# Kernel tuning notes

Hardware: AMD Instinct MI355X
Metric: run time of the kernel (lower is better)

Reference implementation:

```python
import jax, jax.numpy as jnp
import numpy as np
import math

HEADS = 8
DIM_HEAD = 64
EMB = 512
GROUPS = 32
EPS = 100000.0  # module's literal default norm_eps


def setup_inputs() -> dict:
    key = jax.random.key(0)
    ks = jax.random.split(key, 11)
    B, D, H, W = 2, EMB, 64, 64
    s = 1.0 / math.sqrt(EMB)
    inp = {
        "input": jax.random.normal(ks[0], (B, D, H, W), dtype=jnp.float32),
        "gn_gamma": jnp.ones((EMB,), dtype=jnp.float32),
        "gn_beta": jnp.zeros((EMB,), dtype=jnp.float32),
        "wq": jax.random.normal(ks[1], (EMB, EMB), dtype=jnp.float32) * s,
        "bq": jax.random.normal(ks[2], (EMB,), dtype=jnp.float32) * 0.01,
        "wk": jax.random.normal(ks[3], (EMB, EMB), dtype=jnp.float32) * s,
        "bk": jax.random.normal(ks[4], (EMB,), dtype=jnp.float32) * 0.01,
        "wv": jax.random.normal(ks[5], (EMB, EMB), dtype=jnp.float32) * s,
        "bv": jax.random.normal(ks[6], (EMB,), dtype=jnp.float32) * 0.01,
        "wo": jax.random.normal(ks[7], (EMB, EMB), dtype=jnp.float32) * s,
        "bo": jax.random.normal(ks[8], (EMB,), dtype=jnp.float32) * 0.01,
    }
    return inp


def reference(input, gn_gamma, gn_beta, wq, bq, wk, bk, wv, bv, wo, bo):
    B, D, H, W = input.shape
    S = H * W
    residual = input

    # GroupNorm(32, D) over (C/G, H, W) per group, affine per-channel
    xg = input.reshape(B, GROUPS, (D // GROUPS) * H * W)
    mu = jnp.mean(xg, axis=-1, keepdims=True)
    var = jnp.var(xg, axis=-1, keepdims=True)
    xn = (xg - mu) / jnp.sqrt(var + EPS)
    xn = xn.reshape(B, D, H, W) * gn_gamma[:, None, None] + gn_beta[:, None, None]

    # (B, D, H, W) -> (B, S, D)
    x = xn.reshape(B, D, S).transpose(0, 2, 1)

    # projections (torch Linear: y = x @ W.T + b)
    q = (x @ wq.T + bq).reshape(B, S, HEADS, DIM_HEAD).transpose(0, 2, 1, 3)
    k = (x @ wk.T + bk).reshape(B, S, HEADS, DIM_HEAD).transpose(0, 2, 1, 3)
    v = (x @ wv.T + bv).reshape(B, S, HEADS, DIM_HEAD).transpose(0, 2, 1, 3)

    scale = 1.0 / math.sqrt(DIM_HEAD)
    scores = jnp.einsum("bhqd,bhkd->bhqk", q * scale, k)  # [B, h, S, S]
    attn = jax.nn.softmax(scores, axis=-1)
    o = jnp.einsum("bhqk,bhkd->bhqd", attn, v)  # [B, h, S, dh]
    o = o.transpose(0, 2, 1, 3).reshape(B, S, D)

    out = o @ wo.T + bo  # [B, S, D]
    out = out.transpose(0, 2, 1).reshape(B, D, H, W)
    return out + residual
```

## Files before the change

kernel.cpp:

```cpp
#include <hip/hip_runtime.h>

#define EMB 512
#define SEQ 4096
#define BATCH 2
#define NH 8
#define DH 64
#define GN_EPS 100000.0f
#define ALPHA 0.125f

typedef __bf16 bf16;
typedef __bf16 bf16x8 __attribute__((ext_vector_type(8)));
typedef float f32x4 __attribute__((ext_vector_type(4)));

typedef __attribute__((address_space(1))) unsigned int u32g;
typedef __attribute__((address_space(3))) unsigned int u32l;
__device__ __forceinline__ void gll16(const void* g, void* l) {
  __builtin_amdgcn_global_load_lds((const u32g*)g, (u32l*)l, 16, 0, 0);
}

__global__ __launch_bounds__(256) void stats_k(const float* __restrict__ in,
                                               float* __restrict__ rs,
                                               float* __restrict__ ss) {
  const int row = blockIdx.x;
  const float4* p = (const float4*)(in + (size_t)row * SEQ);
  float s = 0.f, s2 = 0.f;
#pragma unroll
  for (int i = 0; i < 4; ++i) {
    float4 v = p[i * 256 + threadIdx.x];
    s += v.x + v.y + v.z + v.w;
    s2 += v.x * v.x + v.y * v.y + v.z * v.z + v.w * v.w;
  }
#pragma unroll
  for (int o = 32; o > 0; o >>= 1) {
    s += __shfl_down(s, o, 64);
    s2 += __shfl_down(s2, o, 64);
  }
  __shared__ float red[8];
  const int wave = threadIdx.x >> 6, lane = threadIdx.x & 63;
  if (lane == 0) { red[wave] = s; red[4 + wave] = s2; }
  __syncthreads();
  if (threadIdx.x == 0) {
    rs[row] = red[0] + red[1] + red[2] + red[3];
    ss[row] = red[4] + red[5] + red[6] + red[7];
  }
}

__global__ __launch_bounds__(256) void gn_fin_k(const float* __restrict__ rs,
                                                const float* __restrict__ ss,
                                                const float* __restrict__ gamma,
                                                const float* __restrict__ beta,
                                                float* __restrict__ sc,
                                                float* __restrict__ tt,
                                                float* __restrict__ xsum) {
  __shared__ float mus[64], rstds[64];
  const int tid = threadIdx.x;
  if (tid < 64) {
    float s = 0.f, s2 = 0.f;
#pragma unroll
    for (int c = 0; c < 16; ++c) { s += rs[tid * 16 + c]; s2 += ss[tid * 16 + c]; }
    float mu = s * (1.f / 65536.f);
    float var = s2 * (1.f / 65536.f) - mu * mu;
    mus[tid] = mu;
    rstds[tid] = rsqrtf(var + GN_EPS);
  }
  __syncthreads();
  for (int idx = tid; idx < BATCH * EMB; idx += 256) {
    int b = idx >> 9, d = idx & 511;
    int g = b * 32 + (d >> 4);
    float s = rstds[g] * gamma[d];
    float t = beta[d] - mus[g] * s;
    sc[idx] = s;
    tt[idx] = t;
    xsum[idx] = s * rs[idx] + 4096.f * t;
  }
}

__global__ __launch_bounds__(256) void wprep_k(const float* __restrict__ wk, const float* __restrict__ wv,
                                               const float* __restrict__ wo,
                                               const float* __restrict__ bv,
                                               const float* __restrict__ xsum,
                                               bf16* __restrict__ wkb, bf16* __restrict__ wvb,
                                               bf16* __restrict__ wob,
                                               float* __restrict__ kxa, float* __restrict__ vsuma) {
  const int wi = blockIdx.y, b = blockIdx.z;
  if (wi == 2 && b == 1) return;
  const float* W = wi == 0 ? wk : wi == 1 ? wv : wo;
  bf16* WO = wi == 0 ? wkb : wi == 1 ? wvb : wob;
  const int tid = threadIdx.x;
  const int n = blockIdx.x * 64 + (tid >> 2);
  const float* Wr = W + (size_t)n * EMB;
  float dot = 0.f;
  const int dq = (tid & 3) * 128;
  for (int d = dq; d < dq + 128; d += 4) {
    float4 w4 = *(const float4*)&Wr[d];
    if (wi < 2) {
      float4 x4 = *(const float4*)&xsum[b * EMB + d];
      dot += w4.x * x4.x + w4.y * x4.y + w4.z * x4.z + w4.w * x4.w;
    }
    if (b == 0) {
      bf16 r[4] = {(bf16)w4.x, (bf16)w4.y, (bf16)w4.z, (bf16)w4.w};
      *(uint2*)&WO[(size_t)n * EMB + d] = *(uint2*)r;
    }
  }
  if (wi < 2) {
    dot += __shfl_xor(dot, 1, 4);
    dot += __shfl_xor(dot, 2, 4);
    if ((tid & 3) == 0) {
      if (wi == 0) kxa[b * EMB + n] = dot;
      else vsuma[b * EMB + n] = dot + 4096.f * bv[n];
    }
  }
}

__global__ __launch_bounds__(256) void wqt_k(const float* __restrict__ wq,
                                             bf16* __restrict__ wqt) {
  __shared__ float t[64][65];
  const int c0 = blockIdx.x * 64, r0 = blockIdx.y * 64;
  const int tid = threadIdx.x;
#pragma unroll
  for (int p = 0; p < 16; ++p) {
    int lin = p * 256 + tid;
    int rl = lin >> 6, cl = lin & 63;
    t[rl][cl] = wq[(size_t)(r0 + rl) * EMB + c0 + cl];
  }
  __syncthreads();
#pragma unroll
  for (int p = 0; p < 16; ++p) {
    int lin = p * 256 + tid;
    int cl = lin >> 6, rl = lin & 63;
    wqt[(size_t)(c0 + cl) * EMB + r0 + rl] = (bf16)t[rl][cl];
  }
}

__global__ __launch_bounds__(256) void nx_k(const float* __restrict__ in,
                                            const float* __restrict__ sc,
                                            const float* __restrict__ tt,
                                            bf16* __restrict__ xds,
                                            bf16* __restrict__ xsd) {
  __shared__ float t[64][65];
  const int s0 = blockIdx.x * 64, d0 = blockIdx.y * 64, b = blockIdx.z;
  const int tid = threadIdx.x;
#pragma unroll
  for (int p = 0; p < 16; ++p) {
    int lin = p * 256 + tid;
    int dl = lin >> 6, sl = lin & 63;
    int d = d0 + dl;
    size_t idx = ((size_t)b * EMB + d) * SEQ + s0 + sl;
    float v = in[idx] * sc[b * EMB + d] + tt[b * EMB + d];
    t[dl][sl] = v;
    xds[idx] = (bf16)v;
  }
  __syncthreads();
#pragma unroll
  for (int p = 0; p < 16; ++p) {
    int lin = p * 256 + tid;
    int sl = lin >> 6, dl = lin & 63;
    xsd[((size_t)b * SEQ + s0 + sl) * EMB + d0 + dl] = (bf16)t[dl][sl];
  }
}

__global__ __launch_bounds__(256) void graw_k(const bf16* __restrict__ xds,
                                              bf16* __restrict__ G) {
  __shared__ __align__(16) bf16 As[64 * 64];
  __shared__ __align__(16) bf16 Bs[64 * 64];
  const int i0 = blockIdx.x * 64, j0 = blockIdx.y * 64, b = blockIdx.z;
  const bf16* X = xds + (size_t)b * EMB * SEQ;
  const int tid = threadIdx.x;
  const int wave = tid >> 6, lane = tid & 63, l16 = lane & 15, quad = lane >> 4;
  const int lr = lane >> 3, lc = (lane & 7) << 3;
  f32x4 acc[4] = {};
  for (int k0 = 0; k0 < SEQ; k0 += 64) {
#pragma unroll
    for (int p = 0; p < 2; ++p) {
      int r = (wave * 2 + p) * 8 + lr;
      gll16(&X[(size_t)(i0 + r) * SEQ + k0 + lc], &As[r * 64 + lc]);
      gll16(&X[(size_t)(j0 + r) * SEQ + k0 + lc], &Bs[r * 64 + lc]);
    }
    __syncthreads();
#pragma unroll
    for (int kt = 0; kt < 2; ++kt) {
      bf16x8 af = *(const bf16x8*)&As[(wave * 16 + l16) * 64 + kt * 32 + quad * 8];
#pragma unroll
      for (int nt = 0; nt < 4; ++nt) {
        bf16x8 bb = *(const bf16x8*)&Bs[(nt * 16 + l16) * 64 + kt * 32 + quad * 8];
        acc[nt] = __builtin_amdgcn_mfma_f32_16x16x32_bf16(af, bb, acc[nt], 0, 0, 0);
      }
    }
    __syncthreads();
  }
#pragma unroll
  for (int nt = 0; nt < 4; ++nt)
#pragma unroll
    for (int r = 0; r < 4; ++r)
      G[((size_t)b * EMB + i0 + wave * 16 + quad * 4 + r) * EMB + j0 + nt * 16 + l16] =
          (bf16)acc[nt][r];
}

__global__ __launch_bounds__(256) void t2_k(const bf16* __restrict__ wkb,
                                            const bf16* __restrict__ G,
                                            bf16* __restrict__ T2) {
  __shared__ __align__(16) bf16 As[64 * 64];
  __shared__ __align__(16) bf16 Bs[64 * 64];
  const int n0 = blockIdx.x * 64, h = blockIdx.y, b = blockIdx.z;
  const int tid = threadIdx.x;
  const int wave = tid >> 6, lane = tid & 63, l16 = lane & 15, quad = lane >> 4;
  const int lr = lane >> 3, lc = (lane & 7) << 3;
  f32x4 acc[4] = {};
  for (int k0 = 0; k0 < EMB; k0 += 64) {
#pragma unroll
    for (int p = 0; p < 2; ++p) {
      int r = (wave * 2 + p) * 8 + lr;
      gll16(&wkb[(size_t)(h * DH + r) * EMB + k0 + lc], &As[r * 64 + lc]);
      gll16(&G[((size_t)b * EMB + n0 + r) * EMB + k0 + lc], &Bs[r * 64 + lc]);
    }
    __syncthreads();
#pragma unroll
    for (int kt = 0; kt < 2; ++kt) {
      bf16x8 af = *(const bf16x8*)&As[(wave * 16 + l16) * 64 + kt * 32 + quad * 8];
#pragma unroll
      for (int nt = 0; nt < 4; ++nt) {
        bf16x8 bb = *(const bf16x8*)&Bs[(nt * 16 + l16) * 64 + kt * 32 + quad * 8];
        acc[nt] = __builtin_amdgcn_mfma_f32_16x16x32_bf16(af, bb, acc[nt], 0, 0, 0);
      }
    }
    __syncthreads();
  }
#pragma unroll
  for (int nt = 0; nt < 4; ++nt)
#pragma unroll
    for (int r = 0; r < 4; ++r)
      T2[((size_t)(b * NH + h) * DH + wave * 16 + quad * 4 + r) * EMB + n0 + nt * 16 + l16] =
          (bf16)acc[nt][r];
}

__global__ __launch_bounds__(256) void mt_k(const bf16* __restrict__ T2,
                                            const bf16* __restrict__ wvb,
                                            const float* __restrict__ bk,
                                            const float* __restrict__ bv,
                                            const float* __restrict__ kxa,
                                            const float* __restrict__ vsuma,
                                            bf16* __restrict__ Pt) {
  __shared__ __align__(16) bf16 As[64 * 64];
  __shared__ __align__(16) bf16 Bs[64 * 64];
  const int bh = blockIdx.x;
  const int b = bh >> 3, h = bh & 7;
  const int tid = threadIdx.x;
  const int wave = tid >> 6, lane = tid & 63, l16 = lane & 15, quad = lane >> 4;
  const int lr = lane >> 3, lc = (lane & 7) << 3;
  f32x4 acc[4] = {};
  for (int k0 = 0; k0 < EMB; k0 += 64) {
#pragma unroll
    for (int p = 0; p < 2; ++p) {
      int r = (wave * 2 + p) * 8 + lr;
      gll16(&T2[((size_t)bh * DH + r) * EMB + k0 + lc], &As[r * 64 + lc]);
      gll16(&wvb[(size_t)(h * DH + r) * EMB + k0 + lc], &Bs[r * 64 + lc]);
    }
    __syncthreads();
#pragma unroll
    for (int kt = 0; kt < 2; ++kt) {
      bf16x8 af = *(const bf16x8*)&As[(wave * 16 + l16) * 64 + kt * 32 + quad * 8];
#pragma unroll
      for (int nt = 0; nt < 4; ++nt) {
        bf16x8 bb = *(const bf16x8*)&Bs[(nt * 16 + l16) * 64 + kt * 32 + quad * 8];
        acc[nt] = __builtin_amdgcn_mfma_f32_16x16x32_bf16(af, bb, acc[nt], 0, 0, 0);
      }
    }
    __syncthreads();
  }
  const float s = ALPHA / 4096.f;
#pragma unroll
  for (int nt = 0; nt < 4; ++nt) {
    int vd = h * DH + nt * 16 + l16;
    float bvv = bv[vd];
    float vxv = vsuma[b * EMB + vd] - 4096.f * bvv;
#pragma unroll
    for (int r = 0; r < 4; ++r) {
      int kdl = wave * 16 + quad * 4 + r;
      int kd = h * DH + kdl;
      float bkv = bk[kd];
      float p = acc[nt][r] + kxa[b * EMB + kd] * bvv + bkv * vxv + 4096.f * bkv * bvv;
      Pt[((size_t)bh * DH + kdl) * DH + nt * 16 + l16] = (bf16)(p * s);
    }
  }
}

__global__ __launch_bounds__(256) void fchain_k(const bf16* __restrict__ wob,
                                                const bf16* __restrict__ Pt,
                                                const bf16* __restrict__ wqt,
                                                bf16* __restrict__ F) {
  __shared__ __align__(16) bf16 Awo[64 * 64];
  __shared__ __align__(16) bf16 Bp[64 * 64];
  __shared__ __align__(16) bf16 Bwq[64 * 64];
  __shared__ __align__(16) bf16 Ps[4 * 16 * 72];
  const int i0 = blockIdx.x * 64, j0 = blockIdx.y * 64, b = blockIdx.z;
  const int tid = threadIdx.x;
  const int wave = tid >> 6, lane = tid & 63, l16 = lane & 15, quad = lane >> 4;
  const int lr = lane >> 3, lc = (lane & 7) << 3;
  bf16* Pw = &Ps[wave * 16 * 72];
  f32x4 accF[4] = {};
  for (int h = 0; h < NH; ++h) {
    __syncthreads();
#pragma unroll
    for (int p = 0; p < 2; ++p) {
      int r = (wave * 2 + p) * 8 + lr;
      gll16(&wob[(size_t)(i0 + r) * EMB + h * DH + lc], &Awo[r * 64 + lc]);
      gll16(&Pt[((size_t)(b * NH + h) * DH + r) * DH + lc], &Bp[r * 64 + lc]);
      gll16(&wqt[(size_t)(j0 + r) * EMB + h * DH + lc], &Bwq[r * 64 + lc]);
    }
    __syncthreads();
    f32x4 at[4] = {};
#pragma unroll
    for (int kt = 0; kt < 2; ++kt) {
      bf16x8 af = *(const bf16x8*)&Awo[(wave * 16 + l16) * 64 + kt * 32 + quad * 8];
#pragma unroll
      for (int nt = 0; nt < 4; ++nt) {
        bf16x8 bb = *(const bf16x8*)&Bp[(nt * 16 + l16) * 64 + kt * 32 + quad * 8];
        at[nt] = __builtin_amdgcn_mfma_f32_16x16x32_bf16(af, bb, at[nt], 0, 0, 0);
      }
    }
#pragma unroll
    for (int nt = 0; nt < 4; ++nt)
#pragma unroll
      for (int r = 0; r < 4; ++r)
        Pw[(quad * 4 + r) * 72 + nt * 16 + l16] = (bf16)at[nt][r];
#pragma unroll
    for (int kt = 0; kt < 2; ++kt) {
      bf16x8 pf = *(const bf16x8*)&Pw[l16 * 72 + kt * 32 + quad * 8];
#pragma unroll
      for (int nt = 0; nt < 4; ++nt) {
        bf16x8 bb = *(const bf16x8*)&Bwq[(nt * 16 + l16) * 64 + kt * 32 + quad * 8];
        accF[nt] = __builtin_amdgcn_mfma_f32_16x16x32_bf16(pf, bb, accF[nt], 0, 0, 0);
      }
    }
  }
#pragma unroll
  for (int nt = 0; nt < 4; ++nt)
#pragma unroll
    for (int r = 0; r < 4; ++r)
      F[((size_t)b * EMB + i0 + wave * 16 + quad * 4 + r) * EMB + j0 + nt * 16 + l16] =
          (bf16)accF[nt][r];
}

__global__ __launch_bounds__(256) void const_k(const float* __restrict__ wo,
                                               const float* __restrict__ bo,
                                               const float* __restrict__ bq,
                                               const float* __restrict__ vsuma,
                                               const bf16* __restrict__ Pt,
                                               float* __restrict__ cst) {
  __shared__ float ycat[512];
  const int i0 = blockIdx.x * 128, b = blockIdx.y;
  const int tid = threadIdx.x;
#pragma unroll
  for (int e = tid; e < 512; e += 256) {
    int h = e >> 6, vd = e & 63;
    float y = vsuma[b * EMB + e] * (1.f / 4096.f);
    const bf16* pp = &Pt[(size_t)(b * NH + h) * DH * DH + vd];
    const float* bqh = &bq[h * DH];
    float acc = 0.f;
#pragma unroll 8
    for (int kd = 0; kd < 64; ++kd) acc += (float)pp[kd * DH] * bqh[kd];
    ycat[e] = y + 4096.f * acc * (1.f / 4096.f) / ALPHA * ALPHA;
  }
  __syncthreads();
  if (tid < 128) {
    int row = i0 + tid;
    const float* wr = &wo[(size_t)row * EMB];
    float acc = 0.f;
    for (int e = 0; e < 512; e += 4) {
      float4 w4 = *(const float4*)&wr[e];
      acc += w4.x * ycat[e] + w4.y * ycat[e + 1] + w4.z * ycat[e + 2] + w4.w * ycat[e + 3];
    }
    cst[b * EMB + row] = bo[row] + acc;
  }
}

__global__ __launch_bounds__(256) void final_k(const bf16* __restrict__ F,
                                               const bf16* __restrict__ xsd,
                                               const float* __restrict__ cst,
                                               const float* __restrict__ in,
                                               float* __restrict__ out) {
  __shared__ __align__(16) bf16 As[128 * 64];
  __shared__ __align__(16) bf16 Bs[64 * 64];
  const int m0 = blockIdx.x * 128, s0 = blockIdx.y * 64, b = blockIdx.z;
  const bf16* Fb = F + (size_t)b * EMB * EMB;
  const bf16* Xb = xsd + (size_t)b * SEQ * EMB;
  const int tid = threadIdx.x;
  const int wave = tid >> 6, lane = tid & 63, l16 = lane & 15, quad = lane >> 4;
  const int lr = lane >> 3, lc = (lane & 7) << 3;
  f32x4 acc[2][4] = {};
  for (int k0 = 0; k0 < EMB; k0 += 64) {
#pragma unroll
    for (int p = 0; p < 4; ++p) {
      int r = (wave * 4 + p) * 8 + lr;
      gll16(&Fb[(size_t)(m0 + r) * EMB + k0 + lc], &As[r * 64 + lc]);
    }
#pragma unroll
    for (int p = 0; p < 2; ++p) {
      int r = (wave * 2 + p) * 8 + lr;
      gll16(&Xb[(size_t)(s0 + r) * EMB + k0 + lc], &Bs[r * 64 + lc]);
    }
    __syncthreads();
#pragma unroll
    for (int kt = 0; kt < 2; ++kt) {
      bf16x8 a0 = *(const bf16x8*)&As[(wave * 32 + l16) * 64 + kt * 32 + quad * 8];
      bf16x8 a1 = *(const bf16x8*)&As[(wave * 32 + 16 + l16) * 64 + kt * 32 + quad * 8];
#pragma unroll
      for (int nt = 0; nt < 4; ++nt) {
        bf16x8 bb = *(const bf16x8*)&Bs[(nt * 16 + l16) * 64 + kt * 32 + quad * 8];
        acc[0][nt] = __builtin_amdgcn_mfma_f32_16x16x32_bf16(a0, bb, acc[0][nt], 0, 0, 0);
        acc[1][nt] = __builtin_amdgcn_mfma_f32_16x16x32_bf16(a1, bb, acc[1][nt], 0, 0, 0);
      }
    }
    __syncthreads();
  }
#pragma unroll
  for (int mt = 0; mt < 2; ++mt) {
    int rowl = m0 + wave * 32 + mt * 16 + quad * 4;
#pragma unroll
    for (int r = 0; r < 4; ++r) {
      float cv = cst[b * EMB + rowl + r];
      size_t base = ((size_t)b * EMB + rowl + r) * SEQ + s0;
#pragma unroll
      for (int nt = 0; nt < 4; ++nt) {
        size_t idx = base + nt * 16 + l16;
        out[idx] = in[idx] + cv + acc[mt][nt][r];
      }
    }
  }
}

extern "C" void kernel_launch(void* const* d_in, const int* in_sizes, int n_in,
                              void* d_out, int out_size, void* d_ws, size_t ws_size,
                              hipStream_t stream) {
  const float* inp = (const float*)d_in[0];
  const float* gam = (const float*)d_in[1];
  const float* bet = (const float*)d_in[2];
  const float* wq = (const float*)d_in[3];
  const float* bq = (const float*)d_in[4];
  const float* wk = (const float*)d_in[5];
  const float* bk = (const float*)d_in[6];
  const float* wv = (const float*)d_in[7];
  const float* bv = (const float*)d_in[8];
  const float* wo = (const float*)d_in[9];
  const float* bo = (const float*)d_in[10];
  float* out = (float*)d_out;
  (void)in_sizes; (void)n_in; (void)out_size; (void)ws_size;

  char* ws = (char*)d_ws;
  size_t off = 0;
  auto take = [&](size_t bytes) -> char* {
    char* p = ws + off;
    off += (bytes + 255) & ~(size_t)255;
    return p;
  };
  float* rs = (float*)take(1024 * 4);
  float* ssq = (float*)take(1024 * 4);
  float* sc = (float*)take(1024 * 4);
  float* tt = (float*)take(1024 * 4);
  float* xsum = (float*)take(1024 * 4);
  float* kxa = (float*)take(1024 * 4);
  float* vsuma = (float*)take(1024 * 4);
  float* cst = (float*)take(1024 * 4);
  const size_t WB = (size_t)EMB * EMB * sizeof(bf16);
  bf16* wkb = (bf16*)take(WB);
  bf16* wvb = (bf16*)take(WB);
  bf16* wob = (bf16*)take(WB);
  bf16* wqtb = (bf16*)take(WB);
  const size_t XB = (size_t)BATCH * SEQ * EMB * sizeof(bf16);
  bf16* xds = (bf16*)take(XB);
  bf16* xsd = (bf16*)take(XB);
  bf16* G = (bf16*)take((size_t)BATCH * EMB * EMB * sizeof(bf16));
  bf16* T2 = (bf16*)take((size_t)BATCH * NH * DH * EMB * sizeof(bf16));
  bf16* Pt = (bf16*)take((size_t)BATCH * NH * DH * DH * sizeof(bf16));
  bf16* F = (bf16*)take((size_t)BATCH * EMB * EMB * sizeof(bf16));

  wqt_k<<<dim3(8, 8), 256, 0, stream>>>(wq, wqtb);
  stats_k<<<1024, 256, 0, stream>>>(inp, rs, ssq);
  gn_fin_k<<<1, 256, 0, stream>>>(rs, ssq, gam, bet, sc, tt, xsum);
  wprep_k<<<dim3(8, 3, 2), 256, 0, stream>>>(wk, wv, wo, bv, xsum, wkb, wvb, wob, kxa, vsuma);
  nx_k<<<dim3(64, 8, 2), 256, 0, stream>>>(inp, sc, tt, xds, xsd);
  graw_k<<<dim3(8, 8, 2), 256, 0, stream>>>(xds, G);
  t2_k<<<dim3(8, 8, 2), 256, 0, stream>>>(wkb, G, T2);
  mt_k<<<16, 256, 0, stream>>>(T2, wvb, bk, bv, kxa, vsuma, Pt);
  fchain_k<<<dim3(8, 8, 2), 256, 0, stream>>>(wob, Pt, wqtb, F);
  const_k<<<dim3(4, 2), 256, 0, stream>>>(wo, bo, bq, vsuma, Pt, cst);
  final_k<<<dim3(4, 64, 2), 256, 0, stream>>>(F, xsd, cst, inp, out);
}
```

Before: 216.8 us.

## Split-K the Gram GEMM, XOR-swizzle LDS tiles, merge weight prep kernels

The X·Xᵀ Gram GEMM had only 128 blocks each looping over the full 4096-long sequence. It is now split eight ways along K into 1024 blocks writing fp32 partials, and a new reduction kernel sums them into bf16. All MFMA kernels now stage LDS tiles with an XOR swizzle on 16-byte chunks to avoid bank conflicts on fragment reads. The weight transpose and weight-prep kernels are merged into one launch that handles both batches per block. The split adds 16 MB of fp32 partial traffic and an extra kernel launch.

```diff
diff --git a/kernel.cpp b/kernel.cpp
--- a/kernel.cpp
+++ b/kernel.cpp
@@ -16,6 +16,14 @@
 typedef __attribute__((address_space(3))) unsigned int u32l;
 __device__ __forceinline__ void gll16(const void* g, void* l) {
   __builtin_amdgcn_global_load_lds((const u32g*)g, (u32l*)l, 16, 0, 0);
+}
+
+__device__ __forceinline__ void stage8(const bf16* g, size_t rowStride, bf16* lds, int lane) {
+  const int r = lane >> 3, cc = (lane & 7) ^ r;
+  gll16(g + (size_t)r * rowStride + cc * 8, lds + lane * 8);
+}
+__device__ __forceinline__ bf16x8 frag(const bf16* lds, int r, int cc) {
+  return *(const bf16x8*)&lds[(((r << 3) + (cc ^ (r & 7))) << 3)];
 }
 
 __global__ __launch_bounds__(256) void stats_k(const float* __restrict__ in,
@@ -75,60 +83,57 @@
   }
 }
 
-__global__ __launch_bounds__(256) void wprep_k(const float* __restrict__ wk, const float* __restrict__ wv,
-                                               const float* __restrict__ wo,
-                                               const float* __restrict__ bv,
-                                               const float* __restrict__ xsum,
-                                               bf16* __restrict__ wkb, bf16* __restrict__ wvb,
-                                               bf16* __restrict__ wob,
-                                               float* __restrict__ kxa, float* __restrict__ vsuma) {
-  const int wi = blockIdx.y, b = blockIdx.z;
-  if (wi == 2 && b == 1) return;
-  const float* W = wi == 0 ? wk : wi == 1 ? wv : wo;
-  bf16* WO = wi == 0 ? wkb : wi == 1 ? wvb : wob;
-  const int tid = threadIdx.x;
-  const int n = blockIdx.x * 64 + (tid >> 2);
-  const float* Wr = W + (size_t)n * EMB;
-  float dot = 0.f;
-  const int dq = (tid & 3) * 128;
-  for (int d = dq; d < dq + 128; d += 4) {
-    float4 w4 = *(const float4*)&Wr[d];
-    if (wi < 2) {
-      float4 x4 = *(const float4*)&xsum[b * EMB + d];
-      dot += w4.x * x4.x + w4.y * x4.y + w4.z * x4.z + w4.w * x4.w;
-    }
-    if (b == 0) {
+__global__ __launch_bounds__(256) void prep_k(const float* __restrict__ wq, const float* __restrict__ wk,
+                                              const float* __restrict__ wv, const float* __restrict__ wo,
+                                              const float* __restrict__ bv,
+                                              const float* __restrict__ xsum,
+                                              bf16* __restrict__ wqt, bf16* __restrict__ wkb,
+                                              bf16* __restrict__ wvb, bf16* __restrict__ wob,
+                                              float* __restrict__ kxa, float* __restrict__ vsuma) {
+  __shared__ float t[64][65];
+  const int y = blockIdx.y, tid = threadIdx.x;
+  if (y < 8) {
+    const int c0 = blockIdx.x * 64, r0 = y * 64;
+#pragma unroll
+    for (int p = 0; p < 16; ++p) {
+      int lin = p * 256 + tid;
+      int rl = lin >> 6, cl = lin & 63;
+      t[rl][cl] = wq[(size_t)(r0 + rl) * EMB + c0 + cl];
+    }
+    __syncthreads();
+#pragma unroll
+    for (int p = 0; p < 16; ++p) {
+      int lin = p * 256 + tid;
+      int cl = lin >> 6, rl = lin & 63;
+      wqt[(size_t)(c0 + cl) * EMB + r0 + rl] = (bf16)t[rl][cl];
+    }
+  } else {
+    const int wi = y - 8;
+    const float* W = wi == 0 ? wk : wi == 1 ? wv : wo;
+    bf16* WO = wi == 0 ? wkb : wi == 1 ? wvb : wob;
+    const int n = blockIdx.x * 64 + (tid >> 2);
+    const float* Wr = W + (size_t)n * EMB;
+    float dot0 = 0.f, dot1 = 0.f;
+    const int dq = (tid & 3) * 128;
+    for (int d = dq; d < dq + 128; d += 4) {
+      float4 w4 = *(const float4*)&Wr[d];
+      if (wi < 2) {
+        float4 x0 = *(const float4*)&xsum[d];
+        float4 x1 = *(const float4*)&xsum[EMB + d];
+        dot0 += w4.x * x0.x + w4.y * x0.y + w4.z * x0.z + w4.w * x0.w;
+        dot1 += w4.x * x1.x + w4.y * x1.y + w4.z * x1.z + w4.w * x1.w;
+      }
       bf16 r[4] = {(bf16)w4.x, (bf16)w4.y, (bf16)w4.z, (bf16)w4.w};
       *(uint2*)&WO[(size_t)n * EMB + d] = *(uint2*)r;
     }
-  }
-  if (wi < 2) {
-    dot += __shfl_xor(dot, 1, 4);
-    dot += __shfl_xor(dot, 2, 4);
-    if ((tid & 3) == 0) {
-      if (wi == 0) kxa[b * EMB + n] = dot;
-      else vsuma[b * EMB + n] = dot + 4096.f * bv[n];
-    }
-  }
-}
-
-__global__ __launch_bounds__(256) void wqt_k(const float* __restrict__ wq,
-                                             bf16* __restrict__ wqt) {
-  __shared__ float t[64][65];
-  const int c0 = blockIdx.x * 64, r0 = blockIdx.y * 64;
-  const int tid = threadIdx.x;
-#pragma unroll
-  for (int p = 0; p < 16; ++p) {
-    int lin = p * 256 + tid;
-    int rl = lin >> 6, cl = lin & 63;
-    t[rl][cl] = wq[(size_t)(r0 + rl) * EMB + c0 + cl];
-  }
-  __syncthreads();
-#pragma unroll
-  for (int p = 0; p < 16; ++p) {
-    int lin = p * 256 + tid;
-    int cl = lin >> 6, rl = lin & 63;
-    wqt[(size_t)(c0 + cl) * EMB + r0 + rl] = (bf16)t[rl][cl];
+    if (wi < 2) {
+      dot0 += __shfl_xor(dot0, 1, 4); dot0 += __shfl_xor(dot0, 2, 4);
+      dot1 += __shfl_xor(dot1, 1, 4); dot1 += __shfl_xor(dot1, 2, 4);
+      if ((tid & 3) == 0) {
+        if (wi == 0) { kxa[n] = dot0; kxa[EMB + n] = dot1; }
+        else { vsuma[n] = dot0 + 4096.f * bv[n]; vsuma[EMB + n] = dot1 + 4096.f * bv[n]; }
+      }
+    }
   }
 }
 
@@ -159,41 +164,52 @@
   }
 }
 
-__global__ __launch_bounds__(256) void graw_k(const bf16* __restrict__ xds,
-                                              bf16* __restrict__ G) {
+__global__ __launch_bounds__(256) void graw2_k(const bf16* __restrict__ xds,
+                                               float* __restrict__ pG) {
   __shared__ __align__(16) bf16 As[64 * 64];
   __shared__ __align__(16) bf16 Bs[64 * 64];
-  const int i0 = blockIdx.x * 64, j0 = blockIdx.y * 64, b = blockIdx.z;
+  const int i0 = (blockIdx.x >> 3) * 64, j0 = (blockIdx.x & 7) * 64;
+  const int kc = blockIdx.y, b = blockIdx.z;
   const bf16* X = xds + (size_t)b * EMB * SEQ;
   const int tid = threadIdx.x;
   const int wave = tid >> 6, lane = tid & 63, l16 = lane & 15, quad = lane >> 4;
-  const int lr = lane >> 3, lc = (lane & 7) << 3;
   f32x4 acc[4] = {};
-  for (int k0 = 0; k0 < SEQ; k0 += 64) {
+  for (int k0 = kc * 512; k0 < kc * 512 + 512; k0 += 64) {
 #pragma unroll
     for (int p = 0; p < 2; ++p) {
-      int r = (wave * 2 + p) * 8 + lr;
-      gll16(&X[(size_t)(i0 + r) * SEQ + k0 + lc], &As[r * 64 + lc]);
-      gll16(&X[(size_t)(j0 + r) * SEQ + k0 + lc], &Bs[r * 64 + lc]);
+      int g = wave * 2 + p;
+      stage8(&X[(size_t)(i0 + g * 8) * SEQ + k0], SEQ, &As[g * 512], lane);
+      stage8(&X[(size_t)(j0 + g * 8) * SEQ + k0], SEQ, &Bs[g * 512], lane);
     }
     __syncthreads();
 #pragma unroll
     for (int kt = 0; kt < 2; ++kt) {
-      bf16x8 af = *(const bf16x8*)&As[(wave * 16 + l16) * 64 + kt * 32 + quad * 8];
-#pragma unroll
-      for (int nt = 0; nt < 4; ++nt) {
-        bf16x8 bb = *(const bf16x8*)&Bs[(nt * 16 + l16) * 64 + kt * 32 + quad * 8];
+      bf16x8 af = frag(As, wave * 16 + l16, kt * 4 + quad);
+#pragma unroll
+      for (int nt = 0; nt < 4; ++nt) {
+        bf16x8 bb = frag(Bs, nt * 16 + l16, kt * 4 + quad);
         acc[nt] = __builtin_amdgcn_mfma_f32_16x16x32_bf16(af, bb, acc[nt], 0, 0, 0);
       }
     }
     __syncthreads();
   }
+  float* pg = pG + ((size_t)(b * 8 + kc) * EMB + i0) * EMB + j0;
 #pragma unroll
   for (int nt = 0; nt < 4; ++nt)
 #pragma unroll
     for (int r = 0; r < 4; ++r)
-      G[((size_t)b * EMB + i0 + wave * 16 + quad * 4 + r) * EMB + j0 + nt * 16 + l16] =
-          (bf16)acc[nt][r];
+      pg[(wave * 16 + quad * 4 + r) * EMB + nt * 16 + l16] = acc[nt][r];
+}
+
+__global__ __launch_bounds__(256) void gsum_k(const float* __restrict__ pG,
+                                              bf16* __restrict__ G) {
+  const int b = blockIdx.x >> 10;
+  const int idx = ((blockIdx.x & 1023) << 8) + threadIdx.x;
+  const float* p = pG + (size_t)b * 8 * 262144 + idx;
+  float s = 0.f;
+#pragma unroll
+  for (int kc = 0; kc < 8; ++kc) s += p[(size_t)kc * 262144];
+  G[(size_t)b * 262144 + idx] = (bf16)s;
 }
 
 __global__ __launch_bounds__(256) void t2_k(const bf16* __restrict__ wkb,
@@ -204,22 +220,21 @@
   const int n0 = blockIdx.x * 64, h = blockIdx.y, b = blockIdx.z;
   const int tid = threadIdx.x;
   const int wave = tid >> 6, lane = tid & 63, l16 = lane & 15, quad = lane >> 4;
-  const int lr = lane >> 3, lc = (lane & 7) << 3;
   f32x4 acc[4] = {};
   for (int k0 = 0; k0 < EMB; k0 += 64) {
 #pragma unroll
     for (int p = 0; p < 2; ++p) {
-      int r = (wave * 2 + p) * 8 + lr;
-      gll16(&wkb[(size_t)(h * DH + r) * EMB + k0 + lc], &As[r * 64 + lc]);
-      gll16(&G[((size_t)b * EMB + n0 + r) * EMB + k0 + lc], &Bs[r * 64 + lc]);
+      int g = wave * 2 + p;
+      stage8(&wkb[(size_t)(h * DH + g * 8) * EMB + k0], EMB, &As[g * 512], lane);
+      stage8(&G[((size_t)b * EMB + n0 + g * 8) * EMB + k0], EMB, &Bs[g * 512], lane);
     }
     __syncthreads();
 #pragma unroll
     for (int kt = 0; kt < 2; ++kt) {
-      bf16x8 af = *(const bf16x8*)&As[(wave * 16 + l16) * 64 + kt * 32 + quad * 8];
-#pragma unroll
-      for (int nt = 0; nt < 4; ++nt) {
-        bf16x8 bb = *(const bf16x8*)&Bs[(nt * 16 + l16) * 64 + kt * 32 + quad * 8];
+      bf16x8 af = frag(As, wave * 16 + l16, kt * 4 + quad);
+#pragma unroll
+      for (int nt = 0; nt < 4; ++nt) {
+        bf16x8 bb = frag(Bs, nt * 16 + l16, kt * 4 + quad);
         acc[nt] = __builtin_amdgcn_mfma_f32_16x16x32_bf16(af, bb, acc[nt], 0, 0, 0);
       }
     }
@@ -246,22 +261,21 @@
   const int b = bh >> 3, h = bh & 7;
   const int tid = threadIdx.x;
   const int wave = tid >> 6, lane = tid & 63, l16 = lane & 15, quad = lane >> 4;
-  const int lr = lane >> 3, lc = (lane & 7) << 3;
   f32x4 acc[4] = {};
   for (int k0 = 0; k0 < EMB; k0 += 64) {
 #pragma unroll
     for (int p = 0; p < 2; ++p) {
-      int r = (wave * 2 + p) * 8 + lr;
-      gll16(&T2[((size_t)bh * DH + r) * EMB + k0 + lc], &As[r * 64 + lc]);
-      gll16(&wvb[(size_t)(h * DH + r) * EMB + k0 + lc], &Bs[r * 64 + lc]);
+      int g = wave * 2 + p;
+      stage8(&T2[((size_t)bh * DH + g * 8) * EMB + k0], EMB, &As[g * 512], lane);
+      stage8(&wvb[(size_t)(h * DH + g * 8) * EMB + k0], EMB, &Bs[g * 512], lane);
     }
     __syncthreads();
 #pragma unroll
     for (int kt = 0; kt < 2; ++kt) {
-      bf16x8 af = *(const bf16x8*)&As[(wave * 16 + l16) * 64 + kt * 32 + quad * 8];
-#pragma unroll
-      for (int nt = 0; nt < 4; ++nt) {
-        bf16x8 bb = *(const bf16x8*)&Bs[(nt * 16 + l16) * 64 + kt * 32 + quad * 8];
+      bf16x8 af = frag(As, wave * 16 + l16, kt * 4 + quad);
+#pragma unroll
+      for (int nt = 0; nt < 4; ++nt) {
+        bf16x8 bb = frag(Bs, nt * 16 + l16, kt * 4 + quad);
         acc[nt] = __builtin_amdgcn_mfma_f32_16x16x32_bf16(af, bb, acc[nt], 0, 0, 0);
       }
     }
@@ -295,26 +309,25 @@
   const int i0 = blockIdx.x * 64, j0 = blockIdx.y * 64, b = blockIdx.z;
   const int tid = threadIdx.x;
   const int wave = tid >> 6, lane = tid & 63, l16 = lane & 15, quad = lane >> 4;
-  const int lr = lane >> 3, lc = (lane & 7) << 3;
   bf16* Pw = &Ps[wave * 16 * 72];
   f32x4 accF[4] = {};
   for (int h = 0; h < NH; ++h) {
     __syncthreads();
 #pragma unroll
     for (int p = 0; p < 2; ++p) {
-      int r = (wave * 2 + p) * 8 + lr;
-      gll16(&wob[(size_t)(i0 + r) * EMB + h * DH + lc], &Awo[r * 64 + lc]);
-      gll16(&Pt[((size_t)(b * NH + h) * DH + r) * DH + lc], &Bp[r * 64 + lc]);
-      gll16(&wqt[(size_t)(j0 + r) * EMB + h * DH + lc], &Bwq[r * 64 + lc]);
+      int g = wave * 2 + p;
+      stage8(&wob[(size_t)(i0 + g * 8) * EMB + h * DH], EMB, &Awo[g * 512], lane);
+      stage8(&Pt[((size_t)(b * NH + h) * DH + g * 8) * DH], DH, &Bp[g * 512], lane);
+      stage8(&wqt[(size_t)(j0 + g * 8) * EMB + h * DH], EMB, &Bwq[g * 512], lane);
     }
     __syncthreads();
     f32x4 at[4] = {};
 #pragma unroll
     for (int kt = 0; kt < 2; ++kt) {
-      bf16x8 af = *(const bf16x8*)&Awo[(wave * 16 + l16) * 64 + kt * 32 + quad * 8];
-#pragma unroll
-      for (int nt = 0; nt < 4; ++nt) {
-        bf16x8 bb = *(const bf16x8*)&Bp[(nt * 16 + l16) * 64 + kt * 32 + quad * 8];
+      bf16x8 af = frag(Awo, wave * 16 + l16, kt * 4 + quad);
+#pragma unroll
+      for (int nt = 0; nt < 4; ++nt) {
+        bf16x8 bb = frag(Bp, nt * 16 + l16, kt * 4 + quad);
         at[nt] = __builtin_amdgcn_mfma_f32_16x16x32_bf16(af, bb, at[nt], 0, 0, 0);
       }
     }
@@ -328,7 +341,7 @@
       bf16x8 pf = *(const bf16x8*)&Pw[l16 * 72 + kt * 32 + quad * 8];
 #pragma unroll
       for (int nt = 0; nt < 4; ++nt) {
-        bf16x8 bb = *(const bf16x8*)&Bwq[(nt * 16 + l16) * 64 + kt * 32 + quad * 8];
+        bf16x8 bb = frag(Bwq, nt * 16 + l16, kt * 4 + quad);
         accF[nt] = __builtin_amdgcn_mfma_f32_16x16x32_bf16(pf, bb, accF[nt], 0, 0, 0);
       }
     }
@@ -359,7 +372,7 @@
     float acc = 0.f;
 #pragma unroll 8
     for (int kd = 0; kd < 64; ++kd) acc += (float)pp[kd * DH] * bqh[kd];
-    ycat[e] = y + 4096.f * acc * (1.f / 4096.f) / ALPHA * ALPHA;
+    ycat[e] = y + acc;
   }
   __syncthreads();
   if (tid < 128) {
@@ -386,27 +399,26 @@
   const bf16* Xb = xsd + (size_t)b * SEQ * EMB;
   const int tid = threadIdx.x;
   const int wave = tid >> 6, lane = tid & 63, l16 = lane & 15, quad = lane >> 4;
-  const int lr = lane >> 3, lc = (lane & 7) << 3;
   f32x4 acc[2][4] = {};
   for (int k0 = 0; k0 < EMB; k0 += 64) {
 #pragma unroll
     for (int p = 0; p < 4; ++p) {
-      int r = (wave * 4 + p) * 8 + lr;
-      gll16(&Fb[(size_t)(m0 + r) * EMB + k0 + lc], &As[r * 64 + lc]);
+      int g = wave * 4 + p;
+      stage8(&Fb[(size_t)(m0 + g * 8) * EMB + k0], EMB, &As[g * 512], lane);
     }
 #pragma unroll
     for (int p = 0; p < 2; ++p) {
-      int r = (wave * 2 + p) * 8 + lr;
-      gll16(&Xb[(size_t)(s0 + r) * EMB + k0 + lc], &Bs[r * 64 + lc]);
+      int g = wave * 2 + p;
+      stage8(&Xb[(size_t)(s0 + g * 8) * EMB + k0], EMB, &Bs[g * 512], lane);
     }
     __syncthreads();
 #pragma unroll
     for (int kt = 0; kt < 2; ++kt) {
-      bf16x8 a0 = *(const bf16x8*)&As[(wave * 32 + l16) * 64 + kt * 32 + quad * 8];
-      bf16x8 a1 = *(const bf16x8*)&As[(wave * 32 + 16 + l16) * 64 + kt * 32 + quad * 8];
-#pragma unroll
-      for (int nt = 0; nt < 4; ++nt) {
-        bf16x8 bb = *(const bf16x8*)&Bs[(nt * 16 + l16) * 64 + kt * 32 + quad * 8];
+      bf16x8 a0 = frag(As, wave * 32 + l16, kt * 4 + quad);
+      bf16x8 a1 = frag(As, wave * 32 + 16 + l16, kt * 4 + quad);
+#pragma unroll
+      for (int nt = 0; nt < 4; ++nt) {
+        bf16x8 bb = frag(Bs, nt * 16 + l16, kt * 4 + quad);
         acc[0][nt] = __builtin_amdgcn_mfma_f32_16x16x32_bf16(a0, bb, acc[0][nt], 0, 0, 0);
         acc[1][nt] = __builtin_amdgcn_mfma_f32_16x16x32_bf16(a1, bb, acc[1][nt], 0, 0, 0);
       }
@@ -469,17 +481,19 @@
   const size_t XB = (size_t)BATCH * SEQ * EMB * sizeof(bf16);
   bf16* xds = (bf16*)take(XB);
   bf16* xsd = (bf16*)take(XB);
+  float* pG = (float*)take((size_t)BATCH * 8 * EMB * EMB * sizeof(float));
   bf16* G = (bf16*)take((size_t)BATCH * EMB * EMB * sizeof(bf16));
   bf16* T2 = (bf16*)take((size_t)BATCH * NH * DH * EMB * sizeof(bf16));
   bf16* Pt = (bf16*)take((size_t)BATCH * NH * DH * DH * sizeof(bf16));
   bf16* F = (bf16*)take((size_t)BATCH * EMB * EMB * sizeof(bf16));
 
-  wqt_k<<<dim3(8, 8), 256, 0, stream>>>(wq, wqtb);
   stats_k<<<1024, 256, 0, stream>>>(inp, rs, ssq);
   gn_fin_k<<<1, 256, 0, stream>>>(rs, ssq, gam, bet, sc, tt, xsum);
-  wprep_k<<<dim3(8, 3, 2), 256, 0, stream>>>(wk, wv, wo, bv, xsum, wkb, wvb, wob, kxa, vsuma);
+  prep_k<<<dim3(8, 11), 256, 0, stream>>>(wq, wk, wv, wo, bv, xsum,
+                                          wqtb, wkb, wvb, wob, kxa, vsuma);
   nx_k<<<dim3(64, 8, 2), 256, 0, stream>>>(inp, sc, tt, xds, xsd);
-  graw_k<<<dim3(8, 8, 2), 256, 0, stream>>>(xds, G);
+  graw2_k<<<dim3(64, 8, 2), 256, 0, stream>>>(xds, pG);
+  gsum_k<<<2048, 256, 0, stream>>>(pG, G);
   t2_k<<<dim3(8, 8, 2), 256, 0, stream>>>(wkb, G, T2);
   mt_k<<<16, 256, 0, stream>>>(T2, wvb, bk, bv, kxa, vsuma, Pt);
   fchain_k<<<dim3(8, 8, 2), 256, 0, stream>>>(wob, Pt, wqtb, F);
```

Measured after the change: 181.3 us. 1.2x faster.
